# Kernel tuning notes

Measured on AMD Instinct MI355X. Metric: run time of the kernel, lower is better.

Reference implementation:

```python
import jax, jax.numpy as jnp
import numpy as np

B, C, H, W = 8, 256, 64, 64
M, R, T_EMB = 4, 4, 128


def conv2d(x, w, b, pad):
    y = jax.lax.conv_general_dilated(x, w, (1, 1), [(pad, pad), (pad, pad)],
                                     dimension_numbers=('NCHW', 'OIHW', 'NCHW'))
    return y + b[None, :, None, None]


def grid_sample_zeros(img, grid):
    # img: [C,H,W]; grid: [...,2]; faithful to torch grid_sample(bilinear,
    # zeros padding, align_corners=True): grid[...,0]->x(width), grid[...,1]->y(height).
    Hh, Ww = img.shape[1], img.shape[2]
    gx = (grid[..., 0] + 1.0) * 0.5 * (Ww - 1)
    gy = (grid[..., 1] + 1.0) * 0.5 * (Hh - 1)
    x0 = jnp.floor(gx); y0 = jnp.floor(gy)
    x1 = x0 + 1.0;      y1 = y0 + 1.0
    wx1 = gx - x0; wx0 = 1.0 - wx1
    wy1 = gy - y0; wy0 = 1.0 - wy1

    def gather(yi, xi):
        valid = (yi >= 0) & (yi < Hh) & (xi >= 0) & (xi < Ww)
        yc = jnp.clip(yi, 0, Hh - 1).astype(jnp.int32)
        xc = jnp.clip(xi, 0, Ww - 1).astype(jnp.int32)
        return img[:, yc, xc] * valid.astype(img.dtype)[None]

    out = (gather(y0, x0) * (wy0 * wx0)[None] + gather(y0, x1) * (wy0 * wx1)[None]
           + gather(y1, x0) * (wy1 * wx0)[None] + gather(y1, x1) * (wy1 * wx1)[None])
    return out  # [C, ...]


def setup_inputs() -> dict:
    key = jax.random.key(0)
    ks = jax.random.split(key, 10)
    s = 0.05
    return {
        'F_x': jax.random.normal(ks[0], (B, C, H, W), jnp.float32),
        'F_c': jax.random.normal(ks[1], (B, C, H, W), jnp.float32),
        't': jax.random.uniform(ks[2], (B,), jnp.float32),
        'w_off': jax.random.normal(ks[3], (2 * M, 2 * C, 3, 3), jnp.float32) * s,
        'b_off': jnp.zeros((2 * M,), jnp.float32),
        'w_attn': jax.random.normal(ks[4], (M, 2 * C, 3, 3), jnp.float32) * s,
        'b_attn': jnp.zeros((M,), jnp.float32),
        'Wp': jnp.ones((M, R), jnp.float32) / R,
        'w_fuse': jax.random.normal(ks[5], (C, M * C, 1, 1), jnp.float32) * s,
        'b_fuse': jnp.zeros((C,), jnp.float32),
        'w1': jax.random.normal(ks[6], (1, T_EMB), jnp.float32) * s,
        'b1': jnp.zeros((T_EMB,), jnp.float32),
        'w2': jax.random.normal(ks[7], (T_EMB, 1), jnp.float32) * s,
        'b2': jnp.zeros((1,), jnp.float32),
    }


def reference(F_x, F_c, t, w_off, b_off, w_attn, b_attn, Wp, w_fuse, b_fuse,
              w1, b1, w2, b2):
    Bb, Cc, Hh, Ww = F_x.shape
    Mm, Rr = Wp.shape
    # interleaved stack/permute/reshape in torch == channel concat [F_x; F_c]
    Fs = jnp.concatenate([F_x, F_c], axis=1)                      # [B,2C,H,W]
    offsets = conv2d(Fs, w_off, b_off, 1).reshape(Bb, Mm, 2, Hh, Ww)
    attn = jax.nn.sigmoid(conv2d(Fs, w_attn, b_attn, 1))          # [B,M,H,W]

    ys = jnp.linspace(-1.0, 1.0, Hh)
    xs = jnp.linspace(-1.0, 1.0, Ww)
    base_grid = jnp.stack(jnp.meshgrid(ys, xs, indexing='ij'), -1)  # [H,W,2] (y,x) order
    # base_pts for R=4 (torch meshgrid ij, rows are (y,x))
    bp = jnp.array([[-0.5, -0.5], [-0.5, 0.5], [0.5, -0.5], [0.5, 0.5]], jnp.float32)
    off = jnp.transpose(offsets, (0, 1, 3, 4, 2))                 # [B,M,H,W,2]
    # grid: [B,M,R,H,W,2]; component order kept as in the original code
    grid = base_grid[None, None, None] + bp[None, None, :, None, None, :] + off[:, :, None]

    # sample F_c per batch over all (M,R,H,W) points at once -> [B,C,M,R,H,W]
    samp = jax.vmap(grid_sample_zeros)(F_c, grid)
    head = jnp.einsum('bcmrhw,mr->bmchw', samp, Wp) * attn[:, :, None]
    head = head.reshape(Bb, Mm * Cc, Hh, Ww)
    F_e = conv2d(head, w_fuse, b_fuse, 0)                         # [B,C,H,W]

    alpha = jax.nn.sigmoid(jax.nn.relu(t[:, None] @ w1 + b1) @ w2 + b2)
    alpha = alpha.reshape(Bb, 1, 1, 1)
    F_out = alpha * F_e + (1.0 - alpha) * F_x
    loss_offset = jnp.mean(jnp.abs(offsets))
    return F_out, loss_offset, offsets
```

## Files before the change

### kernel.cpp

```cpp
#include <hip/hip_runtime.h>
#include <hip/hip_bf16.h>

#define Bc   8
#define Cc   256
#define Hc   64
#define Wc   64
#define HWc  4096
#define KDIM 1024

#define LOSS_IDX   8388608
#define OFFS_BASE  8388609

#define XT_OFF     0u
#define HEAD_OFF   33554432u
#define XF8_OFF    67108864u
#define WBF_OFF    100663296u
#define ATTN_OFF   101187584u
#define ALPHA_OFF  101711872u
#define LOSSP_OFF  101712128u
#define WREP_OFF   101714176u
#define ZPAGE_OFF  101935360u

typedef unsigned short u16;
typedef unsigned char u8;
typedef __attribute__((ext_vector_type(8))) short bf16x8;
typedef __attribute__((ext_vector_type(8))) unsigned short u16x8;
typedef __attribute__((ext_vector_type(4))) float f32x4;
typedef __attribute__((ext_vector_type(2))) float f32x2;

static __device__ __forceinline__ u16 f2bf(float f) {
    unsigned int u = __float_as_uint(f);
    unsigned int r = (u + 0x7FFFu + ((u >> 16) & 1u)) >> 16;
    return (u16)r;
}
static __device__ __forceinline__ float bf2f(u16 h) {
    return __uint_as_float(((unsigned int)h) << 16);
}
static __device__ __forceinline__ unsigned int pk4_fp8(float a, float b, float c, float d) {
    int r = __builtin_amdgcn_cvt_pk_fp8_f32(a, b, 0, false);
    r = __builtin_amdgcn_cvt_pk_fp8_f32(c, d, r, true);
    return (unsigned int)r;
}

__global__ __launch_bounds__(256) void pack_x(const float* __restrict__ Fx,
                                              const float* __restrict__ Fc,
                                              u16* __restrict__ Xt, u16* __restrict__ Xlo,
                                              u8* __restrict__ Xf8) {
    __shared__ float tile[32][33];
    const int blk = blockIdx.x;
    const int b = blk >> 11;
    const int rem = blk & 2047;
    const int hw0 = (rem >> 4) << 5;
    const int c0 = (rem & 15) << 5;
    const int tid = threadIdx.x;
    const int ci = tid >> 5, hwi = tid & 31;
#pragma unroll
    for (int it = 0; it < 4; ++it) {
        const int cc = c0 + ci + it * 8;
        const float* src = (cc < 256) ? Fx + (((size_t)b << 8) + cc) * HWc
                                      : Fc + (((size_t)b << 8) + cc - 256) * HWc;
        tile[ci + it * 8][hwi] = src[hw0 + hwi];
    }
    __syncthreads();
    const int pix = tid >> 3, c4 = (tid & 7) << 2;
    const size_t row = ((size_t)b << 12) + hw0 + pix;
    float v[4];
#pragma unroll
    for (int k = 0; k < 4; ++k) v[k] = tile[c4 + k][pix];
    ushort4 hi4, lo4;
#pragma unroll
    for (int k = 0; k < 4; ++k) {
        const u16 h = f2bf(v[k]);
        ((u16*)&hi4)[k] = h;
        ((u16*)&lo4)[k] = f2bf(v[k] - bf2f(h));
    }
    *(ushort4*)(Xt + row * 512 + c0 + c4) = hi4;
    *(ushort4*)(Xlo + row * 512 + c0 + c4) = lo4;
    if (c0 >= 256) {
        *(unsigned int*)(Xf8 + row * 256 + (c0 - 256) + c4) = pk4_fp8(v[0], v[1], v[2], v[3]);
    }
}

__global__ __launch_bounds__(256) void prep(const float* __restrict__ wf,
                                            u8* __restrict__ wf8,
                                            const float* __restrict__ w_off,
                                            const float* __restrict__ w_attn,
                                            u16* __restrict__ wconv,
                                            float* __restrict__ zpage) {
    const int tid = threadIdx.x;
    if (blockIdx.x < 256) {
        const int i = blockIdx.x * 256 + tid;
        const float4 v = *(const float4*)(wf + (size_t)i * 4);
        *(unsigned int*)(wf8 + (size_t)i * 4) = pk4_fp8(v.x, v.y, v.z, v.w);
    } else if (blockIdx.x < 264) {
        const int step = blockIdx.x - 256;
        for (int n = tid; n < 1728; n += 256) {
            const int par = n & 1;
            const int slot = (n >> 1) & 3;
            const int pair = (n >> 3) % 6;
            const int tap = (n / 48) % 9;
            const int prec = (n / 432) & 1;
            const int sub = n / 864;
            const int oc = pair * 2 + par;
            const int c = slot ^ (pair & 3);
            const int ch = step * 64 + sub * 32 + c * 8;
            u16x8 out;
#pragma unroll
            for (int j = 0; j < 8; ++j) {
                const float v = (oc < 8)
                    ? w_off[((size_t)oc * 512 + ch + j) * 9 + tap]
                    : w_attn[((size_t)(oc - 8) * 512 + ch + j) * 9 + tap];
                const u16 h = f2bf(v);
                out[j] = prec ? f2bf(v - bf2f(h)) : h;
            }
            *(u16x8*)(wconv + ((size_t)step * 1728 + n) * 8) = out;
        }
    } else {
        if (tid < 64) zpage[tid] = 0.f;
    }
}

#define XBUF_STR 67584
#define XPRC_STR 33792
#define XROW_STR 8448
#define B_BASE   135168
__global__ __launch_bounds__(512) void conv_mfma(
    const u16* __restrict__ Xt, const u16* __restrict__ Xlo,
    const u16* __restrict__ wconv, const float* __restrict__ zpage,
    const float* __restrict__ b_off, const float* __restrict__ b_attn,
    float* __restrict__ dout, float* __restrict__ attnb, float* __restrict__ lossp) {
    __shared__ char smem[163840];

    const int tid = threadIdx.x;
    const int wv = tid >> 6, lane = tid & 63;
    const int gp = wv >> 2, qd = wv & 3;
    const int l15 = lane & 15, g = lane >> 4;
    const int b = blockIdx.x >> 5;
    const int h0 = (blockIdx.x & 31) * 2;
    const int wrow = qd >> 1, wcol0 = (qd & 1) * 32;

    if (tid < 256) {
        const int bu = tid >> 7, pr = (tid >> 6) & 1, rr = (tid >> 4) & 3;
        const int hp = (tid >> 3) & 1, cc = tid & 7;
        const int p = hp ? 65 : 0;
        const float4 z = {0.f, 0.f, 0.f, 0.f};
        *(float4*)(smem + bu * XBUF_STR + pr * XPRC_STR + rr * XROW_STR + p * 128 + cc * 16) = z;
    }

    int pre[2][3];
#pragma unroll
    for (int f = 0; f < 2; ++f)
#pragma unroll
        for (int dx = 0; dx < 3; ++dx) {
            const int p = wcol0 + f * 16 + l15 + dx;
            pre[f][dx] = wrow * XROW_STR + p * 128 + ((((gp << 2) | g) ^ (p & 7)) << 4);
        }
    const int bpair = l15 >> 1, bpar = l15 & 1;
    const int vb = B_BASE + gp * 13824 + bpair * 128 + ((g ^ (bpair & 3)) << 5) + bpar * 16;

    auto stage_X = [&](int step, int buf) {
#pragma unroll
        for (int k = 0; k < 9; ++k) {
            const int f = wv * 9 + k;
            const int prec = f / 36, rr = (f / 9) & 3, i = f % 9;
            const int p = i * 8 + (lane >> 3);
            const int c = (lane & 7) ^ (p & 7);
            const int col = p - 1;
            const int h = h0 - 1 + rr;
            const bool act = (p >= 1) && (p <= 64);
            const u16* srcb = prec ? Xlo : Xt;
            const char* gsrc = (h >= 0 && h < 64)
                ? (const char*)(srcb + (((size_t)((b << 12) + h * 64 + col)) << 9) + step * 64 + c * 8)
                : (const char*)zpage + ((lane & 7) << 4);
            char* ldst = smem + buf * XBUF_STR + prec * XPRC_STR + rr * XROW_STR + i * 1024;
            if (act)
                __builtin_amdgcn_global_load_lds(
                    (const __attribute__((address_space(1))) unsigned int*)gsrc,
                    (__attribute__((address_space(3))) unsigned int*)ldst, 16, 0, 0);
        }
    };
    auto stage_B = [&](int step) {
        for (int i = wv; i < 27; i += 8) {
            const char* gsrc = (const char*)wconv + (((size_t)step * 1728) + i * 64 + lane) * 16;
            char* ldst = smem + B_BASE + i * 1024;
            __builtin_amdgcn_global_load_lds(
                (const __attribute__((address_space(1))) unsigned int*)gsrc,
                (__attribute__((address_space(3))) unsigned int*)ldst, 16, 0, 0);
        }
    };

    __syncthreads();
    stage_X(0, 0);
    stage_B(0);
    __syncthreads();

    f32x4 acc0 = {}, acc1 = {};

    for (int step = 0; step < 8; ++step) {
        if (step < 7) {
            stage_X(step + 1, (step + 1) & 1);
            asm volatile("s_waitcnt vmcnt(9)" ::: "memory");
        } else {
            asm volatile("s_waitcnt vmcnt(0)" ::: "memory");
        }
        __builtin_amdgcn_s_barrier();
        __builtin_amdgcn_sched_barrier(0);

#pragma unroll
        for (int tap = 0; tap < 9; ++tap) {
            const int dy = tap / 3, dx = tap % 3;
            const bf16x8 bh = *(const bf16x8*)(smem + vb + tap * 768);
            const bf16x8 bl = *(const bf16x8*)(smem + vb + 6912 + tap * 768);
            const bf16x8 a0h = *(const bf16x8*)(smem + pre[0][dx] + dy * XROW_STR);
            const bf16x8 a1h = *(const bf16x8*)(smem + pre[1][dx] + dy * XROW_STR);
            const bf16x8 a0l = *(const bf16x8*)(smem + pre[0][dx] + XPRC_STR + dy * XROW_STR);
            const bf16x8 a1l = *(const bf16x8*)(smem + pre[1][dx] + XPRC_STR + dy * XROW_STR);
            acc0 = __builtin_amdgcn_mfma_f32_16x16x32_bf16(a0h, bh, acc0, 0, 0, 0);
            acc1 = __builtin_amdgcn_mfma_f32_16x16x32_bf16(a1h, bh, acc1, 0, 0, 0);
            acc0 = __builtin_amdgcn_mfma_f32_16x16x32_bf16(a0h, bl, acc0, 0, 0, 0);
            acc1 = __builtin_amdgcn_mfma_f32_16x16x32_bf16(a1h, bl, acc1, 0, 0, 0);
            acc0 = __builtin_amdgcn_mfma_f32_16x16x32_bf16(a0l, bh, acc0, 0, 0, 0);
            acc1 = __builtin_amdgcn_mfma_f32_16x16x32_bf16(a1l, bh, acc1, 0, 0, 0);
        }

        __builtin_amdgcn_sched_barrier(0);
        __builtin_amdgcn_s_barrier();
        __builtin_amdgcn_sched_barrier(0);
        if (step < 7) stage_B(step + 1);
        const int d = (step & 1) ? -XBUF_STR : XBUF_STR;
#pragma unroll
        for (int f = 0; f < 2; ++f)
#pragma unroll
            for (int dx = 0; dx < 3; ++dx) pre[f][dx] += d;
    }

    __syncthreads();
    float* eL = (float*)smem;
    if (l15 < 12) {
#pragma unroll
        for (int r = 0; r < 4; ++r) {
            const int px0 = wrow * 64 + wcol0 + g * 4 + r;
            eL[(gp * 12 + l15) * 128 + px0] = acc0[r];
            eL[(gp * 12 + l15) * 128 + px0 + 16] = acc1[r];
        }
    }
    __syncthreads();
    float labs = 0.f;
    if (tid < 256) {
        const int oc = tid >> 5, seg = tid & 31;
        const float4 v0 = *(const float4*)&eL[oc * 128 + seg * 4];
        const float4 v1 = *(const float4*)&eL[(12 + oc) * 128 + seg * 4];
        const float bo = b_off[oc];
        float4 o;
        o.x = v0.x + v1.x + bo; o.y = v0.y + v1.y + bo;
        o.z = v0.z + v1.z + bo; o.w = v0.w + v1.w + bo;
        *(float4*)(dout + OFFS_BASE + (((size_t)b * 8 + oc) << 12) + h0 * 64 + seg * 4) = o;
        labs = fabsf(o.x) + fabsf(o.y) + fabsf(o.z) + fabsf(o.w);
    } else if (tid < 384) {
        const int t2 = tid - 256;
        const int oc = t2 >> 5, seg = t2 & 31;
        const float4 v0 = *(const float4*)&eL[(8 + oc) * 128 + seg * 4];
        const float4 v1 = *(const float4*)&eL[(20 + oc) * 128 + seg * 4];
        const float ba = b_attn[oc];
        float4 o;
        o.x = 1.f / (1.f + expf(-(v0.x + v1.x + ba)));
        o.y = 1.f / (1.f + expf(-(v0.y + v1.y + ba)));
        o.z = 1.f / (1.f + expf(-(v0.z + v1.z + ba)));
        o.w = 1.f / (1.f + expf(-(v0.w + v1.w + ba)));
        *(float4*)(attnb + (((size_t)b * 4 + (oc)) << 12) + h0 * 64 + seg * 4) = o;
    }
#pragma unroll
    for (int off = 32; off; off >>= 1) labs += __shfl_down(labs, off);
    float* wr = (float*)(smem + 14336);
    if (lane == 0) wr[wv] = labs;
    __syncthreads();
    if (tid == 0) {
        float s = 0.f;
#pragma unroll
        for (int i = 0; i < 8; ++i) s += wr[i];
        lossp[blockIdx.x] = s;
    }
}

__global__ __launch_bounds__(256) void finalize_small(
    const float* __restrict__ lossp, const float* __restrict__ t,
    const float* __restrict__ w1, const float* __restrict__ b1,
    const float* __restrict__ w2, const float* __restrict__ b2,
    float* __restrict__ dout, float* __restrict__ alpha) {
    __shared__ float sd[4];
    const int tid = threadIdx.x;
    float s = lossp[tid];
#pragma unroll
    for (int off = 32; off; off >>= 1) s += __shfl_down(s, off);
    if ((tid & 63) == 0) sd[tid >> 6] = s;
    __syncthreads();
    if (tid == 0) dout[LOSS_IDX] = (sd[0] + sd[1] + sd[2] + sd[3]) * (1.f / 262144.f);

    for (int b = 0; b < 8; ++b) {
        __syncthreads();
        float v = 0.f;
        if (tid < 128) v = fmaxf(fmaf(t[b], w1[tid], b1[tid]), 0.f) * w2[tid];
#pragma unroll
        for (int off = 32; off; off >>= 1) v += __shfl_down(v, off);
        if ((tid & 63) == 0) sd[tid >> 6] = v;
        __syncthreads();
        if (tid == 0) alpha[b] = 1.f / (1.f + expf(-(sd[0] + sd[1] + b2[0])));
    }
}

__global__ __launch_bounds__(256) void sample_head(
    const u8* __restrict__ Xf8, const float* __restrict__ dout,
    const float* __restrict__ attnb, const float* __restrict__ Wp,
    u8* __restrict__ head) {
    const int tid = threadIdx.x;
    const int wv = tid >> 6, lane = tid & 63;
    const int item = blockIdx.x * 4 + wv;
    const int b = item >> 14;
    const int m = (item >> 12) & 3;
    const int p = item & 4095;
    const int h = p >> 6, wc = p & 63;
    const int hl = lane >> 5, l32 = lane & 31;

    const float off0 = dout[OFFS_BASE + (((size_t)b * 8 + 2 * m) << 12) + p];
    const float off1 = dout[OFFS_BASE + (((size_t)b * 8 + 2 * m + 1) << 12) + p];
    const float a    = attnb[(((size_t)b * 4 + m) << 12) + p];

    const float ysh = -1.f + h * (2.f / 63.f);
    const float xsw = -1.f + wc * (2.f / 63.f);

    const u8* base = Xf8 + (((size_t)b << 12) << 8) + l32 * 8;
    float acc[8] = {};

#pragma unroll
    for (int r = 0; r < 4; ++r) {
        const float bpy = (r < 2) ? -0.5f : 0.5f;
        const float bpx = (r & 1) ? 0.5f : -0.5f;
        const float c0 = ysh + bpy + off0;
        const float c1 = xsw + bpx + off1;
        const float ix = (c0 + 1.f) * 31.5f;
        const float iy = (c1 + 1.f) * 31.5f;
        const float x0 = floorf(ix), y0 = floorf(iy);
        const float wx1 = ix - x0, wx0 = 1.f - wx1;
        const float wy1 = iy - y0, wy0 = 1.f - wy1;
        const float xf = x0 + hl;
        const float wxl = (hl ? wx1 : wx0) * (Wp[m * 4 + r] * a);
        const bool xin = (xf >= 0.f) && (xf < 64.f);
        const bool v0 = xin && (y0 >= 0.f) && (y0 < 64.f);
        const bool v1 = xin && (y0 >= -1.f) && (y0 < 63.f);
        const int xi = (int)xf;
        uint2 u0, u1;
        if (v0) u0 = *(const uint2*)(base + ((size_t)((((int)y0) << 6) + xi)) * 256);
        if (v1) u1 = *(const uint2*)(base + ((size_t)((((int)y0 + 1) << 6) + xi)) * 256);
        if (v0) {
            const float w = wxl * wy0;
            const f32x2 pa = __builtin_amdgcn_cvt_pk_f32_fp8((int)u0.x, false);
            const f32x2 pb = __builtin_amdgcn_cvt_pk_f32_fp8((int)u0.x, true);
            const f32x2 pc = __builtin_amdgcn_cvt_pk_f32_fp8((int)u0.y, false);
            const f32x2 pd = __builtin_amdgcn_cvt_pk_f32_fp8((int)u0.y, true);
            acc[0] = fmaf(w, pa[0], acc[0]); acc[1] = fmaf(w, pa[1], acc[1]);
            acc[2] = fmaf(w, pb[0], acc[2]); acc[3] = fmaf(w, pb[1], acc[3]);
            acc[4] = fmaf(w, pc[0], acc[4]); acc[5] = fmaf(w, pc[1], acc[5]);
            acc[6] = fmaf(w, pd[0], acc[6]); acc[7] = fmaf(w, pd[1], acc[7]);
        }
        if (v1) {
            const float w = wxl * wy1;
            const f32x2 pa = __builtin_amdgcn_cvt_pk_f32_fp8((int)u1.x, false);
            const f32x2 pb = __builtin_amdgcn_cvt_pk_f32_fp8((int)u1.x, true);
            const f32x2 pc = __builtin_amdgcn_cvt_pk_f32_fp8((int)u1.y, false);
            const f32x2 pd = __builtin_amdgcn_cvt_pk_f32_fp8((int)u1.y, true);
            acc[0] = fmaf(w, pa[0], acc[0]); acc[1] = fmaf(w, pa[1], acc[1]);
            acc[2] = fmaf(w, pb[0], acc[2]); acc[3] = fmaf(w, pb[1], acc[3]);
            acc[4] = fmaf(w, pc[0], acc[4]); acc[5] = fmaf(w, pc[1], acc[5]);
            acc[6] = fmaf(w, pd[0], acc[6]); acc[7] = fmaf(w, pd[1], acc[7]);
        }
    }
#pragma unroll
    for (int j = 0; j < 8; ++j) acc[j] += __shfl_xor(acc[j], 32);
    if (lane < 32) {
        uint2 o;
        o.x = pk4_fp8(acc[0], acc[1], acc[2], acc[3]);
        o.y = pk4_fp8(acc[4], acc[5], acc[6], acc[7]);
        *(uint2*)(head + ((((size_t)b << 12) + p)) * KDIM + m * 256 + l32 * 8) = o;
    }
}

__global__ __launch_bounds__(256) void fuse_gemm(
    const u8* __restrict__ head, const u8* __restrict__ wf8,
    const float* __restrict__ Fx, const float* __restrict__ bfuse,
    const float* __restrict__ alpha, float* __restrict__ dout) {
    __shared__ __attribute__((aligned(16))) char smem[2][2][8192];

    const int tid = threadIdx.x;
    const int lane = tid & 63, wv = tid >> 6;
    const int wm = wv >> 1, wn = wv & 1;
    const int l15 = lane & 15, g = lane >> 4;
    const size_t arow0 = (size_t)blockIdx.x * 128;
    const int co0 = blockIdx.y * 128;

    f32x4 acc[4][4] = {};

    const int isB = wv >> 1;
    const int whalf = wv & 1;
    const u8* srcbase = isB ? wf8 + (size_t)co0 * KDIM : head + arow0 * KDIM;

    auto stage = [&](int kt, int buf) {
#pragma unroll
        for (int i = 0; i < 4; ++i) {
            const int row = whalf * 64 + i * 16 + (lane >> 2);
            const int gq = (lane & 3) ^ ((row >> 1) & 3);
            const u8* gsrc = srcbase + (size_t)row * KDIM + kt * 64 + gq * 16;
            char* ldst = smem[buf][isB] + (whalf * 64 + i * 16) * 64;
            __builtin_amdgcn_global_load_lds(
                (const __attribute__((address_space(1))) unsigned int*)gsrc,
                (__attribute__((address_space(3))) unsigned int*)ldst, 16, 0, 0);
        }
    };

    stage(0, 0);
    __syncthreads();

    for (int kt = 0; kt < 16; ++kt) {
        if (kt < 15) {
            stage(kt + 1, (kt + 1) & 1);
            asm volatile("s_waitcnt vmcnt(4)" ::: "memory");
        } else {
            asm volatile("s_waitcnt vmcnt(0)" ::: "memory");
        }
        __builtin_amdgcn_s_barrier();
        __builtin_amdgcn_sched_barrier(0);

        const char* Ab = smem[kt & 1][0];
        const char* Bb = smem[kt & 1][1];
#pragma unroll
        for (int s = 0; s < 2; ++s) {
            const int gg = s * 4 + g;
            long av[4], bv[4];
#pragma unroll
            for (int f = 0; f < 4; ++f) {
                const int ra = wm * 64 + f * 16 + l15;
                const int rb = wn * 64 + f * 16 + l15;
                const int sa = (gg >> 1) ^ ((ra >> 1) & 3);
                const int sb = (gg >> 1) ^ ((rb >> 1) & 3);
                av[f] = *(const long*)(Ab + ra * 64 + sa * 16 + (gg & 1) * 8);
                bv[f] = *(const long*)(Bb + rb * 64 + sb * 16 + (gg & 1) * 8);
            }
#pragma unroll
            for (int i = 0; i < 4; ++i)
#pragma unroll
                for (int j = 0; j < 4; ++j)
                    acc[i][j] = __builtin_amdgcn_mfma_f32_16x16x32_fp8_fp8(av[i], bv[j], acc[i][j], 0, 0, 0);
        }

        __builtin_amdgcn_sched_barrier(0);
        __builtin_amdgcn_s_barrier();
        __builtin_amdgcn_sched_barrier(0);
    }

    const int b = (int)(arow0 >> 12);
    const float al = alpha[b], il = 1.f - al;
    const int pixbase = (int)(arow0 & 4095);
#pragma unroll
    for (int i = 0; i < 4; ++i) {
        const int rowl = wm * 64 + i * 16 + g * 4;
        const int pix = pixbase + rowl;
#pragma unroll
        for (int j = 0; j < 4; ++j) {
            const int co = co0 + wn * 64 + j * 16 + l15;
            const float bias = bfuse[co];
            const size_t idx = (((size_t)b << 8) + co) * HWc + pix;
            const float4 fx = *(const float4*)(Fx + idx);
            const f32x4 v = acc[i][j];
            float4 o;
            o.x = al * (v[0] + bias) + il * fx.x;
            o.y = al * (v[1] + bias) + il * fx.y;
            o.z = al * (v[2] + bias) + il * fx.z;
            o.w = al * (v[3] + bias) + il * fx.w;
            *(float4*)(dout + idx) = o;
        }
    }
}

extern "C" void kernel_launch(void* const* d_in, const int* in_sizes, int n_in,
                              void* d_out, int out_size, void* d_ws, size_t ws_size,
                              hipStream_t stream) {
    const float* F_x    = (const float*)d_in[0];
    const float* F_c    = (const float*)d_in[1];
    const float* t      = (const float*)d_in[2];
    const float* w_off  = (const float*)d_in[3];
    const float* b_off  = (const float*)d_in[4];
    const float* w_attn = (const float*)d_in[5];
    const float* b_attn = (const float*)d_in[6];
    const float* Wp     = (const float*)d_in[7];
    const float* w_fuse = (const float*)d_in[8];
    const float* b_fuse = (const float*)d_in[9];
    const float* w1     = (const float*)d_in[10];
    const float* b1     = (const float*)d_in[11];
    const float* w2     = (const float*)d_in[12];
    const float* b2     = (const float*)d_in[13];
    float* out = (float*)d_out;

    char* ws = (char*)d_ws;
    u16*   Xt    = (u16*)(ws + XT_OFF);
    u16*   Xlo   = (u16*)(ws + HEAD_OFF);
    u8*    head8 = (u8*)(ws + HEAD_OFF);
    u8*    Xf8   = (u8*)(ws + XF8_OFF);
    u8*    wf8   = (u8*)(ws + WBF_OFF);
    float* attnb = (float*)(ws + ATTN_OFF);
    float* alphb = (float*)(ws + ALPHA_OFF);
    float* lossp = (float*)(ws + LOSSP_OFF);
    u16*   wconv = (u16*)(ws + WREP_OFF);
    float* zpage = (float*)(ws + ZPAGE_OFF);

    pack_x<<<dim3(16384), dim3(256), 0, stream>>>(F_x, F_c, Xt, Xlo, Xf8);
    prep<<<dim3(265), dim3(256), 0, stream>>>(w_fuse, wf8, w_off, w_attn, wconv, zpage);
    conv_mfma<<<dim3(256), dim3(512), 0, stream>>>(Xt, Xlo, wconv, zpage, b_off, b_attn,
                                                   out, attnb, lossp);
    finalize_small<<<dim3(1), dim3(256), 0, stream>>>(lossp, t, w1, b1, w2, b2, out, alphb);
    sample_head<<<dim3(32768), dim3(256), 0, stream>>>(Xf8, out, attnb, Wp, head8);
    fuse_gemm<<<dim3(256, 2), dim3(256), 0, stream>>>(head8, wf8, F_x, b_fuse, alphb, out);
}
```

Before: 126.5 us.

## Store conv residual input as scaled FP8 and merge prep into pack kernel

```diff
diff --git a/kernel.cpp b/kernel.cpp
--- a/kernel.cpp
+++ b/kernel.cpp
@@ -14,6 +14,7 @@
 #define XT_OFF     0u
 #define HEAD_OFF   33554432u
 #define XF8_OFF    67108864u
+#define WC8_OFF    75497472u
 #define WBF_OFF    100663296u
 #define ATTN_OFF   101187584u
 #define ALPHA_OFF  101711872u
@@ -28,6 +29,10 @@
 typedef __attribute__((ext_vector_type(4))) float f32x4;
 typedef __attribute__((ext_vector_type(2))) float f32x2;
 
+#define GLL(gsrc, ldst) __builtin_amdgcn_global_load_lds( \
+    (const __attribute__((address_space(1))) unsigned int*)(gsrc), \
+    (__attribute__((address_space(3))) unsigned int*)(ldst), 16, 0, 0)
+
 static __device__ __forceinline__ u16 f2bf(float f) {
     unsigned int u = __float_as_uint(f);
     unsigned int r = (u + 0x7FFFu + ((u >> 16) & 1u)) >> 16;
@@ -42,58 +47,50 @@
     return (unsigned int)r;
 }
 
-__global__ __launch_bounds__(256) void pack_x(const float* __restrict__ Fx,
-                                              const float* __restrict__ Fc,
-                                              u16* __restrict__ Xt, u16* __restrict__ Xlo,
-                                              u8* __restrict__ Xf8) {
-    __shared__ float tile[32][33];
-    const int blk = blockIdx.x;
-    const int b = blk >> 11;
-    const int rem = blk & 2047;
-    const int hw0 = (rem >> 4) << 5;
-    const int c0 = (rem & 15) << 5;
+__global__ __launch_bounds__(256) void pack_x(
+    const float* __restrict__ Fx, const float* __restrict__ Fc,
+    u16* __restrict__ Xt, u8* __restrict__ Xlo8, u8* __restrict__ Xf8,
+    const float* __restrict__ wf, u8* __restrict__ wf8,
+    const float* __restrict__ w_off, const float* __restrict__ w_attn,
+    u16* __restrict__ wconv, u8* __restrict__ wconv8, float* __restrict__ zpage) {
     const int tid = threadIdx.x;
-    const int ci = tid >> 5, hwi = tid & 31;
-#pragma unroll
-    for (int it = 0; it < 4; ++it) {
-        const int cc = c0 + ci + it * 8;
-        const float* src = (cc < 256) ? Fx + (((size_t)b << 8) + cc) * HWc
-                                      : Fc + (((size_t)b << 8) + cc - 256) * HWc;
-        tile[ci + it * 8][hwi] = src[hw0 + hwi];
-    }
-    __syncthreads();
-    const int pix = tid >> 3, c4 = (tid & 7) << 2;
-    const size_t row = ((size_t)b << 12) + hw0 + pix;
-    float v[4];
-#pragma unroll
-    for (int k = 0; k < 4; ++k) v[k] = tile[c4 + k][pix];
-    ushort4 hi4, lo4;
-#pragma unroll
-    for (int k = 0; k < 4; ++k) {
-        const u16 h = f2bf(v[k]);
-        ((u16*)&hi4)[k] = h;
-        ((u16*)&lo4)[k] = f2bf(v[k] - bf2f(h));
-    }
-    *(ushort4*)(Xt + row * 512 + c0 + c4) = hi4;
-    *(ushort4*)(Xlo + row * 512 + c0 + c4) = lo4;
-    if (c0 >= 256) {
-        *(unsigned int*)(Xf8 + row * 256 + (c0 - 256) + c4) = pk4_fp8(v[0], v[1], v[2], v[3]);
-    }
-}
-
-__global__ __launch_bounds__(256) void prep(const float* __restrict__ wf,
-                                            u8* __restrict__ wf8,
-                                            const float* __restrict__ w_off,
-                                            const float* __restrict__ w_attn,
-                                            u16* __restrict__ wconv,
-                                            float* __restrict__ zpage) {
-    const int tid = threadIdx.x;
-    if (blockIdx.x < 256) {
-        const int i = blockIdx.x * 256 + tid;
+    if (blockIdx.x < 16384) {
+        __shared__ float tile[32][33];
+        const int blk = blockIdx.x;
+        const int b = blk >> 11;
+        const int rem = blk & 2047;
+        const int hw0 = (rem >> 4) << 5;
+        const int c0 = (rem & 15) << 5;
+        const int ci = tid >> 5, hwi = tid & 31;
+#pragma unroll
+        for (int it = 0; it < 4; ++it) {
+            const int cc = c0 + ci + it * 8;
+            const float* src = (cc < 256) ? Fx + (((size_t)b << 8) + cc) * HWc
+                                          : Fc + (((size_t)b << 8) + cc - 256) * HWc;
+            tile[ci + it * 8][hwi] = src[hw0 + hwi];
+        }
+        __syncthreads();
+        const int pix = tid >> 3, c4 = (tid & 7) << 2;
+        const size_t row = ((size_t)b << 12) + hw0 + pix;
+        float v[4], lo[4];
+        ushort4 hi4;
+#pragma unroll
+        for (int k = 0; k < 4; ++k) {
+            v[k] = tile[c4 + k][pix];
+            const u16 h = f2bf(v[k]);
+            ((u16*)&hi4)[k] = h;
+            lo[k] = (v[k] - bf2f(h)) * 256.f;
+        }
+        *(ushort4*)(Xt + row * 512 + c0 + c4) = hi4;
+        *(unsigned int*)(Xlo8 + row * 512 + c0 + c4) = pk4_fp8(lo[0], lo[1], lo[2], lo[3]);
+        if (c0 >= 256)
+            *(unsigned int*)(Xf8 + row * 256 + (c0 - 256) + c4) = pk4_fp8(v[0], v[1], v[2], v[3]);
+    } else if (blockIdx.x < 16640) {
+        const int i = (blockIdx.x - 16384) * 256 + tid;
         const float4 v = *(const float4*)(wf + (size_t)i * 4);
         *(unsigned int*)(wf8 + (size_t)i * 4) = pk4_fp8(v.x, v.y, v.z, v.w);
-    } else if (blockIdx.x < 264) {
-        const int step = blockIdx.x - 256;
+    } else if (blockIdx.x < 16648) {
+        const int step = blockIdx.x - 16640;
         for (int n = tid; n < 1728; n += 256) {
             const int par = n & 1;
             const int slot = (n >> 1) & 3;
@@ -115,21 +112,35 @@
             }
             *(u16x8*)(wconv + ((size_t)step * 1728 + n) * 8) = out;
         }
+        for (int n = tid; n < 1152; n += 256) {
+            const int slot = n & 3;
+            const int oc = (n >> 2) & 15;
+            const int tap = (n >> 6) % 9;
+            const int sub = n / 576;
+            const int g = slot ^ (oc >> 2);
+            const int ch = step * 64 + sub * 32 + g * 8;
+            float v[8];
+#pragma unroll
+            for (int j = 0; j < 8; ++j)
+                v[j] = (oc < 8) ? w_off[((size_t)oc * 512 + ch + j) * 9 + tap]
+                     : (oc < 12) ? w_attn[((size_t)(oc - 8) * 512 + ch + j) * 9 + tap] : 0.f;
+            uint2 o;
+            o.x = pk4_fp8(v[0], v[1], v[2], v[3]);
+            o.y = pk4_fp8(v[4], v[5], v[6], v[7]);
+            *(uint2*)(wconv8 + (size_t)step * 9216 + n * 8) = o;
+        }
     } else {
         if (tid < 64) zpage[tid] = 0.f;
     }
 }
 
-#define XBUF_STR 67584
-#define XPRC_STR 33792
-#define XROW_STR 8448
-#define B_BASE   135168
 __global__ __launch_bounds__(512) void conv_mfma(
-    const u16* __restrict__ Xt, const u16* __restrict__ Xlo,
-    const u16* __restrict__ wconv, const float* __restrict__ zpage,
+    const u16* __restrict__ Xt, const u8* __restrict__ Xlo8,
+    const u16* __restrict__ wconv, const u8* __restrict__ wconv8,
+    const float* __restrict__ zpage,
     const float* __restrict__ b_off, const float* __restrict__ b_attn,
     float* __restrict__ dout, float* __restrict__ attnb, float* __restrict__ lossp) {
-    __shared__ char smem[163840];
+    __shared__ char smem[138240];
 
     const int tid = threadIdx.x;
     const int wv = tid >> 6, lane = tid & 63;
@@ -139,53 +150,72 @@
     const int h0 = (blockIdx.x & 31) * 2;
     const int wrow = qd >> 1, wcol0 = (qd & 1) * 32;
 
-    if (tid < 256) {
-        const int bu = tid >> 7, pr = (tid >> 6) & 1, rr = (tid >> 4) & 3;
-        const int hp = (tid >> 3) & 1, cc = tid & 7;
-        const int p = hp ? 65 : 0;
+    if (tid < 192) {
         const float4 z = {0.f, 0.f, 0.f, 0.f};
-        *(float4*)(smem + bu * XBUF_STR + pr * XPRC_STR + rr * XROW_STR + p * 128 + cc * 16) = z;
-    }
-
-    int pre[2][3];
+        if (tid < 128) {
+            const int bu = tid >> 6, rr = (tid >> 4) & 3, hp = (tid >> 3) & 1, cc = tid & 7;
+            *(float4*)(smem + bu * 33792 + rr * 8448 + (hp ? 65 : 0) * 128 + cc * 16) = z;
+        } else {
+            const int t2 = tid - 128;
+            const int bu = t2 >> 5, rr = (t2 >> 3) & 3, hp = (t2 >> 2) & 1, cc = t2 & 3;
+            *(float4*)(smem + 67584 + bu * 16896 + rr * 4224 + (hp ? 65 : 0) * 64 + cc * 16) = z;
+        }
+    }
+
+    int pre[2][3], plo[2][3];
 #pragma unroll
     for (int f = 0; f < 2; ++f)
 #pragma unroll
         for (int dx = 0; dx < 3; ++dx) {
             const int p = wcol0 + f * 16 + l15 + dx;
-            pre[f][dx] = wrow * XROW_STR + p * 128 + ((((gp << 2) | g) ^ (p & 7)) << 4);
+            pre[f][dx] = wrow * 8448 + p * 128 + ((((gp << 2) | g) ^ (p & 7)) << 4);
+            const int cl = (gp * 2 + (g >> 1)) ^ ((p & 3) ^ ((p >> 2) & 3));
+            plo[f][dx] = 67584 + wrow * 4224 + p * 64 + cl * 16 + (g & 1) * 8;
         }
     const int bpair = l15 >> 1, bpar = l15 & 1;
-    const int vb = B_BASE + gp * 13824 + bpair * 128 + ((g ^ (bpair & 3)) << 5) + bpar * 16;
+    const int vb = 101376 + gp * 13824 + bpair * 128 + ((g ^ (bpair & 3)) << 5) + bpar * 16;
+    const int vb8 = 129024 + gp * 4608 + l15 * 32 + ((g ^ (l15 >> 2)) << 3);
 
     auto stage_X = [&](int step, int buf) {
 #pragma unroll
-        for (int k = 0; k < 9; ++k) {
-            const int f = wv * 9 + k;
-            const int prec = f / 36, rr = (f / 9) & 3, i = f % 9;
-            const int p = i * 8 + (lane >> 3);
-            const int c = (lane & 7) ^ (p & 7);
-            const int col = p - 1;
-            const int h = h0 - 1 + rr;
-            const bool act = (p >= 1) && (p <= 64);
-            const u16* srcb = prec ? Xlo : Xt;
-            const char* gsrc = (h >= 0 && h < 64)
-                ? (const char*)(srcb + (((size_t)((b << 12) + h * 64 + col)) << 9) + step * 64 + c * 8)
-                : (const char*)zpage + ((lane & 7) << 4);
-            char* ldst = smem + buf * XBUF_STR + prec * XPRC_STR + rr * XROW_STR + i * 1024;
-            if (act)
-                __builtin_amdgcn_global_load_lds(
-                    (const __attribute__((address_space(1))) unsigned int*)gsrc,
-                    (__attribute__((address_space(3))) unsigned int*)ldst, 16, 0, 0);
+        for (int k = 0; k < 7; ++k) {
+            const int f = wv * 7 + k;
+            if (f < 36) {
+                const int rr = f / 9, i = f % 9;
+                const int p = i * 8 + (lane >> 3);
+                const int c = (lane & 7) ^ (p & 7);
+                const int h = h0 - 1 + rr;
+                const bool act = (p >= 1) && (p <= 64);
+                const char* gsrc = (h >= 0 && h < 64)
+                    ? (const char*)(Xt + (((size_t)((b << 12) + h * 64 + p - 1)) << 9) + step * 64 + c * 8)
+                    : (const char*)zpage + ((lane & 7) << 4);
+                char* ldst = smem + buf * 33792 + rr * 8448 + i * 1024;
+                if (act) GLL(gsrc, ldst);
+            } else {
+                const int f2 = f - 36;
+                const int rr = f2 / 5, i = f2 % 5;
+                const int p = i * 16 + (lane >> 2);
+                const int c = (lane & 3) ^ ((p & 3) ^ ((p >> 2) & 3));
+                const int h = h0 - 1 + rr;
+                const bool act = (p >= 1) && (p <= 64);
+                const char* gsrc = (h >= 0 && h < 64)
+                    ? (const char*)(Xlo8 + (((size_t)((b << 12) + h * 64 + p - 1)) << 9) + step * 64 + c * 16)
+                    : (const char*)zpage + ((lane & 3) << 4);
+                char* ldst = smem + 67584 + buf * 16896 + rr * 4224 + i * 1024;
+                if (act) GLL(gsrc, ldst);
+            }
         }
     };
     auto stage_B = [&](int step) {
-        for (int i = wv; i < 27; i += 8) {
-            const char* gsrc = (const char*)wconv + (((size_t)step * 1728) + i * 64 + lane) * 16;
-            char* ldst = smem + B_BASE + i * 1024;
-            __builtin_amdgcn_global_load_lds(
-                (const __attribute__((address_space(1))) unsigned int*)gsrc,
-                (__attribute__((address_space(3))) unsigned int*)ldst, 16, 0, 0);
+        for (int i = wv; i < 36; i += 8) {
+            if (i < 27) {
+                const char* gsrc = (const char*)wconv + (((size_t)step * 1728) + i * 64 + lane) * 16;
+                GLL(gsrc, smem + 101376 + i * 1024);
+            } else {
+                const int j = i - 27;
+                const char* gsrc = (const char*)wconv8 + (size_t)step * 9216 + j * 1024 + lane * 16;
+                GLL(gsrc, smem + 129024 + j * 1024);
+            }
         }
     };
 
@@ -194,12 +224,12 @@
     stage_B(0);
     __syncthreads();
 
-    f32x4 acc0 = {}, acc1 = {};
+    f32x4 acc0 = {}, acc1 = {}, al0 = {}, al1 = {};
 
     for (int step = 0; step < 8; ++step) {
         if (step < 7) {
             stage_X(step + 1, (step + 1) & 1);
-            asm volatile("s_waitcnt vmcnt(9)" ::: "memory");
+            asm volatile("s_waitcnt vmcnt(7)" ::: "memory");
         } else {
             asm volatile("s_waitcnt vmcnt(0)" ::: "memory");
         }
@@ -211,27 +241,29 @@
             const int dy = tap / 3, dx = tap % 3;
             const bf16x8 bh = *(const bf16x8*)(smem + vb + tap * 768);
             const bf16x8 bl = *(const bf16x8*)(smem + vb + 6912 + tap * 768);
-            const bf16x8 a0h = *(const bf16x8*)(smem + pre[0][dx] + dy * XROW_STR);
-            const bf16x8 a1h = *(const bf16x8*)(smem + pre[1][dx] + dy * XROW_STR);
-            const bf16x8 a0l = *(const bf16x8*)(smem + pre[0][dx] + XPRC_STR + dy * XROW_STR);
-            const bf16x8 a1l = *(const bf16x8*)(smem + pre[1][dx] + XPRC_STR + dy * XROW_STR);
+            const long b8 = *(const long*)(smem + vb8 + tap * 512);
+            const bf16x8 a0h = *(const bf16x8*)(smem + pre[0][dx] + dy * 8448);
+            const bf16x8 a1h = *(const bf16x8*)(smem + pre[1][dx] + dy * 8448);
+            const long a0l = *(const long*)(smem + plo[0][dx] + dy * 4224);
+            const long a1l = *(const long*)(smem + plo[1][dx] + dy * 4224);
             acc0 = __builtin_amdgcn_mfma_f32_16x16x32_bf16(a0h, bh, acc0, 0, 0, 0);
             acc1 = __builtin_amdgcn_mfma_f32_16x16x32_bf16(a1h, bh, acc1, 0, 0, 0);
             acc0 = __builtin_amdgcn_mfma_f32_16x16x32_bf16(a0h, bl, acc0, 0, 0, 0);
             acc1 = __builtin_amdgcn_mfma_f32_16x16x32_bf16(a1h, bl, acc1, 0, 0, 0);
-            acc0 = __builtin_amdgcn_mfma_f32_16x16x32_bf16(a0l, bh, acc0, 0, 0, 0);
-            acc1 = __builtin_amdgcn_mfma_f32_16x16x32_bf16(a1l, bh, acc1, 0, 0, 0);
+            al0 = __builtin_amdgcn_mfma_f32_16x16x32_fp8_fp8(a0l, b8, al0, 0, 0, 0);
+            al1 = __builtin_amdgcn_mfma_f32_16x16x32_fp8_fp8(a1l, b8, al1, 0, 0, 0);
         }
 
         __builtin_amdgcn_sched_barrier(0);
         __builtin_amdgcn_s_barrier();
         __builtin_amdgcn_sched_barrier(0);
         if (step < 7) stage_B(step + 1);
-        const int d = (step & 1) ? -XBUF_STR : XBUF_STR;
+        const int dh = (step & 1) ? -33792 : 33792;
+        const int dl = (step & 1) ? -16896 : 16896;
 #pragma unroll
         for (int f = 0; f < 2; ++f)
 #pragma unroll
-            for (int dx = 0; dx < 3; ++dx) pre[f][dx] += d;
+            for (int dx = 0; dx < 3; ++dx) { pre[f][dx] += dh; plo[f][dx] += dl; }
     }
 
     __syncthreads();
@@ -240,8 +272,8 @@
 #pragma unroll
         for (int r = 0; r < 4; ++r) {
             const int px0 = wrow * 64 + wcol0 + g * 4 + r;
-            eL[(gp * 12 + l15) * 128 + px0] = acc0[r];
-            eL[(gp * 12 + l15) * 128 + px0 + 16] = acc1[r];
+            eL[(gp * 12 + l15) * 128 + px0] = acc0[r] + al0[r] * (1.f / 256.f);
+            eL[(gp * 12 + l15) * 128 + px0 + 16] = acc1[r] + al1[r] * (1.f / 256.f);
         }
     }
     __syncthreads();
@@ -267,7 +299,7 @@
         o.y = 1.f / (1.f + expf(-(v0.y + v1.y + ba)));
         o.z = 1.f / (1.f + expf(-(v0.z + v1.z + ba)));
         o.w = 1.f / (1.f + expf(-(v0.w + v1.w + ba)));
-        *(float4*)(attnb + (((size_t)b * 4 + (oc)) << 12) + h0 * 64 + seg * 4) = o;
+        *(float4*)(attnb + (((size_t)b * 4 + oc) << 12) + h0 * 64 + seg * 4) = o;
     }
 #pragma unroll
     for (int off = 32; off; off >>= 1) labs += __shfl_down(labs, off);
@@ -410,9 +442,7 @@
             const int gq = (lane & 3) ^ ((row >> 1) & 3);
             const u8* gsrc = srcbase + (size_t)row * KDIM + kt * 64 + gq * 16;
             char* ldst = smem[buf][isB] + (whalf * 64 + i * 16) * 64;
-            __builtin_amdgcn_global_load_lds(
-                (const __attribute__((address_space(1))) unsigned int*)gsrc,
-                (__attribute__((address_space(3))) unsigned int*)ldst, 16, 0, 0);
+            GLL(gsrc, ldst);
         }
     };
 
@@ -500,21 +530,23 @@
     float* out = (float*)d_out;
 
     char* ws = (char*)d_ws;
-    u16*   Xt    = (u16*)(ws + XT_OFF);
-    u16*   Xlo   = (u16*)(ws + HEAD_OFF);
-    u8*    head8 = (u8*)(ws + HEAD_OFF);
-    u8*    Xf8   = (u8*)(ws + XF8_OFF);
-    u8*    wf8   = (u8*)(ws + WBF_OFF);
-    float* attnb = (float*)(ws + ATTN_OFF);
-    float* alphb = (float*)(ws + ALPHA_OFF);
-    float* lossp = (float*)(ws + LOSSP_OFF);
-    u16*   wconv = (u16*)(ws + WREP_OFF);
-    float* zpage = (float*)(ws + ZPAGE_OFF);
-
-    pack_x<<<dim3(16384), dim3(256), 0, stream>>>(F_x, F_c, Xt, Xlo, Xf8);
-    prep<<<dim3(265), dim3(256), 0, stream>>>(w_fuse, wf8, w_off, w_attn, wconv, zpage);
-    conv_mfma<<<dim3(256), dim3(512), 0, stream>>>(Xt, Xlo, wconv, zpage, b_off, b_attn,
-                                                   out, attnb, lossp);
+    u16*   Xt     = (u16*)(ws + XT_OFF);
+    u8*    Xlo8   = (u8*)(ws + HEAD_OFF);
+    u8*    head8  = (u8*)(ws + HEAD_OFF);
+    u8*    Xf8    = (u8*)(ws + XF8_OFF);
+    u8*    wconv8 = (u8*)(ws + WC8_OFF);
+    u8*    wf8    = (u8*)(ws + WBF_OFF);
+    float* attnb  = (float*)(ws + ATTN_OFF);
+    float* alphb  = (float*)(ws + ALPHA_OFF);
+    float* lossp  = (float*)(ws + LOSSP_OFF);
+    u16*   wconv  = (u16*)(ws + WREP_OFF);
+    float* zpage  = (float*)(ws + ZPAGE_OFF);
+
+    pack_x<<<dim3(16649), dim3(256), 0, stream>>>(F_x, F_c, Xt, Xlo8, Xf8,
+                                                  w_fuse, wf8, w_off, w_attn,
+                                                  wconv, wconv8, zpage);
+    conv_mfma<<<dim3(256), dim3(512), 0, stream>>>(Xt, Xlo8, wconv, wconv8, zpage,
+                                                   b_off, b_attn, out, attnb, lossp);
     finalize_small<<<dim3(1), dim3(256), 0, stream>>>(lossp, t, w1, b1, w2, b2, out, alphb);
     sample_head<<<dim3(32768), dim3(256), 0, stream>>>(Xf8, out, attnb, Wp, head8);
     fuse_gemm<<<dim3(256, 2), dim3(256), 0, stream>>>(head8, wf8, F_x, b_fuse, alphb, out);
```

Result: no change. 128.4 us (+1.5%).
